# Kernel optimization log

Hardware: AMD Instinct MI355X
Metric: run time of the kernel (lower is better)

## Reference

```python
import jax, jax.numpy as jnp
import numpy as np

N_NODES = 50000
N_EDGES = 640000
IN_FEATS = 512
HID = 128
OUT_FEATS = 128
N_GRAPHS = 256


def setup_inputs() -> dict:
    key = jax.random.key(0)
    ks = jax.random.split(key, 7)
    x = jax.random.normal(ks[0], (N_NODES, IN_FEATS), dtype=jnp.float32)
    edge_index = jax.random.randint(ks[1], (2, N_EDGES), 0, N_NODES, dtype=jnp.int32)
    batch = jnp.sort(jax.random.randint(ks[2], (N_NODES,), 0, N_GRAPHS, dtype=jnp.int32))
    W1 = jax.random.normal(ks[3], (IN_FEATS, HID), dtype=jnp.float32) * (1.0 / np.sqrt(IN_FEATS))
    b1 = jnp.zeros((HID,), jnp.float32)
    W2 = jax.random.normal(ks[4], (HID, OUT_FEATS), dtype=jnp.float32) * (1.0 / np.sqrt(HID))
    b2 = jnp.zeros((OUT_FEATS,), jnp.float32)
    return {"x": x, "W1": W1, "b1": b1, "W2": W2, "b2": b2,
            "edge_index": edge_index, "batch": batch}


def reference(x, W1, b1, W2, b2, edge_index, batch):
    N = x.shape[0]
    loop = jnp.arange(N, dtype=edge_index.dtype)
    # PyG GCNConv default: add self-loops, symmetric deg^-1/2 normalization
    row = jnp.concatenate([edge_index[0], loop])  # source
    col = jnp.concatenate([edge_index[1], loop])  # target
    deg = jax.ops.segment_sum(jnp.ones_like(col, x.dtype), col, num_segments=N)
    dinv = jnp.where(deg > 0, jax.lax.rsqrt(deg), 0.0)
    norm = dinv[row] * dinv[col]  # [E+N]

    def gcn_conv(h, W, b):
        h = h @ W  # linear transform first (PyG order)
        msg = h[row] * norm[:, None]  # gather + scale
        agg = jax.ops.segment_sum(msg, col, num_segments=N)  # scatter-add
        return agg + b

    h = jax.nn.relu(gcn_conv(x, W1, b1))  # dropout is identity in eval mode
    h = gcn_conv(h, W2, b2)
    hs = jax.ops.segment_sum(h, batch, num_segments=N_GRAPHS)  # global_add_pool
    return hs, h
```

## Files before the change

kernel.cpp:

```cpp
#include <hip/hip_runtime.h>
#include <hip/hip_bf16.h>

#define N_NODES  50000
#define N_EDGES  640000
#define IN_FEATS 512
#define HID      128
#define OUT_FEATS 128
#define N_GRAPHS 256

#define SCAN_CHUNK 1024
#define SCAN_BLOCKS ((N_NODES + SCAN_CHUNK - 1) / SCAN_CHUNK)

typedef __attribute__((ext_vector_type(8))) short short8;
typedef __attribute__((ext_vector_type(4))) float f32x4;

__device__ __forceinline__ float bf2f(unsigned u16) {
    return __uint_as_float(u16 << 16);
}
__device__ __forceinline__ unsigned short f2bf(float f) {
    __hip_bfloat16 h = __float2bfloat16(f);
    return *(unsigned short*)&h;
}

#define PREP_BLOCKS 840

__global__ __launch_bounds__(256) void k_prep(const float* __restrict__ W1,
                                              const float* __restrict__ W2,
                                              const int* __restrict__ batch,
                                              unsigned short* __restrict__ wt1,
                                              unsigned short* __restrict__ wt2,
                                              int* __restrict__ cnt,
                                              int* __restrict__ gstart,
                                              float* __restrict__ hs) {
    int b = blockIdx.x;
    int t = threadIdx.x;
    if (b < 196) {
        int i = b * 256 + t;
        if (i < N_NODES) {
            int bt = batch[i];
            int bp = (i == 0) ? -1 : batch[i - 1];
            for (int g = bp + 1; g <= bt; ++g) gstart[g] = i;
            if (i == N_NODES - 1)
                for (int g = bt + 1; g <= N_GRAPHS; ++g) gstart[g] = N_NODES;
        }
    } else if (b < 392) {
        int i = (b - 196) * 256 + t;
        if (i < N_NODES) cnt[i] = 0;
    } else if (b < 648) {
        int idx = (b - 392) * 256 + t;
        int n = idx & 127, k = idx >> 7;
        wt1[(size_t)n * IN_FEATS + k] = f2bf(W1[(size_t)k * 128 + n]);
    } else if (b < 712) {
        int idx = (b - 648) * 256 + t;
        int n = idx & 127, k = idx >> 7;
        wt2[(size_t)n * HID + k] = f2bf(W2[(size_t)k * 128 + n]);
    } else {
        int idx = (b - 712) * 256 + t;
        hs[idx] = 0.f;
    }
}


__global__ void k_count(const int* __restrict__ col, int* __restrict__ cnt) {
    int e4 = (blockIdx.x * blockDim.x + threadIdx.x) * 4;
    if (e4 >= N_EDGES) return;
    int4 c = *(const int4*)(col + e4);
    atomicAdd(&cnt[c.x], 1);
    atomicAdd(&cnt[c.y], 1);
    atomicAdd(&cnt[c.z], 1);
    atomicAdd(&cnt[c.w], 1);
}

__global__ __launch_bounds__(256) void k_scan_a(const int* __restrict__ cnt,
                                                int* __restrict__ offs,
                                                int* __restrict__ bsum) {
    __shared__ int sums[256];
    int t = threadIdx.x;
    int base = blockIdx.x * SCAN_CHUNK + t * 4;
    int c0 = 0, c1 = 0, c2 = 0, c3 = 0;
    if (base + 3 < N_NODES) {
        int4 v = *(const int4*)(cnt + base);
        c0 = v.x; c1 = v.y; c2 = v.z; c3 = v.w;
    } else {
        if (base + 0 < N_NODES) c0 = cnt[base + 0];
        if (base + 1 < N_NODES) c1 = cnt[base + 1];
        if (base + 2 < N_NODES) c2 = cnt[base + 2];
    }
    int ts = c0 + c1 + c2 + c3;
    sums[t] = ts;
    __syncthreads();
#pragma unroll
    for (int off = 1; off < 256; off <<= 1) {
        int add = (t >= off) ? sums[t - off] : 0;
        __syncthreads();
        sums[t] += add;
        __syncthreads();
    }
    int ex = sums[t] - ts;
    if (base + 3 < N_NODES) {
        int4 o;
        o.x = ex; o.y = ex + c0; o.z = ex + c0 + c1; o.w = ex + c0 + c1 + c2;
        *(int4*)(offs + base) = o;
    } else {
        if (base + 0 < N_NODES) offs[base + 0] = ex;
        if (base + 1 < N_NODES) offs[base + 1] = ex + c0;
        if (base + 2 < N_NODES) offs[base + 2] = ex + c0 + c1;
    }
    if (t == 255) bsum[blockIdx.x] = sums[255];
}

__global__ __launch_bounds__(256) void k_scan_c(const int* __restrict__ cnt,
                                                const int* __restrict__ bsum,
                                                int* __restrict__ offs,
                                                int* __restrict__ cursor,
                                                float* __restrict__ dinv) {
    __shared__ int sb[64];
    int t = threadIdx.x;
    int b = blockIdx.x;
    if (t < 64) sb[t] = (t < SCAN_BLOCKS) ? bsum[t] : 0;
    __syncthreads();
#pragma unroll
    for (int off = 1; off < 64; off <<= 1) {
        int add = 0;
        if (t < 64 && t >= off) add = sb[t - off];
        __syncthreads();
        if (t < 64) sb[t] += add;
        __syncthreads();
    }
    int add = (b == 0) ? 0 : sb[b - 1];
    int base = b * SCAN_CHUNK + t * 4;
    if (base + 3 < N_NODES) {
        int4 o = *(const int4*)(offs + base);
        o.x += add; o.y += add; o.z += add; o.w += add;
        *(int4*)(offs + base) = o;
        *(int4*)(cursor + base) = o;
        int4 c = *(const int4*)(cnt + base);
        float4 d;
        d.x = rsqrtf((float)c.x + 1.0f);
        d.y = rsqrtf((float)c.y + 1.0f);
        d.z = rsqrtf((float)c.z + 1.0f);
        d.w = rsqrtf((float)c.w + 1.0f);
        *(float4*)(dinv + base) = d;
    } else {
#pragma unroll
        for (int j = 0; j < 4; ++j) {
            int i = base + j;
            if (i < N_NODES) {
                int o = offs[i] + add;
                offs[i] = o; cursor[i] = o;
                dinv[i] = rsqrtf((float)cnt[i] + 1.0f);
            }
        }
    }
    if (b == 0 && t == 0) offs[N_NODES] = N_EDGES;
}

__global__ void k_fill(const int* __restrict__ row, const int* __restrict__ col,
                       int* __restrict__ cursor, int* __restrict__ srcIdx) {
    int e4 = (blockIdx.x * blockDim.x + threadIdx.x) * 4;
    if (e4 >= N_EDGES) return;
    int4 r = *(const int4*)(row + e4);
    int4 c = *(const int4*)(col + e4);
    srcIdx[atomicAdd(&cursor[c.x], 1)] = r.x;
    srcIdx[atomicAdd(&cursor[c.y], 1)] = r.y;
    srcIdx[atomicAdd(&cursor[c.z], 1)] = r.z;
    srcIdx[atomicAdd(&cursor[c.w], 1)] = r.w;
}


template <int K>
__global__ __launch_bounds__(256) void k_gemm1(const float* __restrict__ A,
                                               const unsigned short* __restrict__ Bt,
                                               unsigned short* __restrict__ Cb, int M) {
    __shared__ unsigned short As[4][128][8];
    __shared__ unsigned short Bs[4][128][8];
    int tid = threadIdx.x;
    int wave = tid >> 6;
    int lane = tid & 63;
    int quad = lane >> 4;
    int l15 = lane & 15;
    int m0 = blockIdx.x * 128;
    int mw = (wave >> 1) * 64;
    int nw = (wave & 1) * 64;

    f32x4 acc[4][4];
#pragma unroll
    for (int i = 0; i < 4; ++i)
#pragma unroll
        for (int j = 0; j < 4; ++j) acc[i][j] = (f32x4){0.f, 0.f, 0.f, 0.f};

    int r0s = tid >> 2, kq0 = tid & 3;
    int r1s = r0s + 64;
    int gm0 = m0 + r0s; if (gm0 >= M) gm0 = M - 1;
    int gm1 = m0 + r1s; if (gm1 >= M) gm1 = M - 1;
    const float* ap0 = A + (size_t)gm0 * K + kq0 * 8;
    const float* ap1 = A + (size_t)gm1 * K + kq0 * 8;

    for (int k0 = 0; k0 < K; k0 += 32) {
        {
            float4 v0 = *(const float4*)(ap0 + k0);
            float4 v1 = *(const float4*)(ap0 + k0 + 4);
            float f[8] = {v0.x, v0.y, v0.z, v0.w, v1.x, v1.y, v1.z, v1.w};
            short8 pk;
#pragma unroll
            for (int j = 0; j < 8; ++j) pk[j] = (short)f2bf(f[j]);
            *(short8*)&As[kq0][r0s][0] = pk;
            v0 = *(const float4*)(ap1 + k0);
            v1 = *(const float4*)(ap1 + k0 + 4);
            float g[8] = {v0.x, v0.y, v0.z, v0.w, v1.x, v1.y, v1.z, v1.w};
#pragma unroll
            for (int j = 0; j < 8; ++j) pk[j] = (short)f2bf(g[j]);
            *(short8*)&As[kq0][r1s][0] = pk;
        }
#pragma unroll
        for (int i = 0; i < 2; ++i) {
            int slot = tid + i * 256;
            int n = slot >> 2, kq = slot & 3;
            *(short8*)&Bs[kq][n][0] = *(const short8*)(Bt + (size_t)n * K + k0 + kq * 8);
        }
        __syncthreads();
        short8 af[4], bfr[4];
#pragma unroll
        for (int i = 0; i < 4; ++i) af[i] = *(short8*)&As[quad][mw + i * 16 + l15][0];
#pragma unroll
        for (int j = 0; j < 4; ++j) bfr[j] = *(short8*)&Bs[quad][nw + j * 16 + l15][0];
#pragma unroll
        for (int i = 0; i < 4; ++i)
#pragma unroll
            for (int j = 0; j < 4; ++j)
                acc[i][j] = __builtin_amdgcn_mfma_f32_16x16x32_bf16(af[i], bfr[j], acc[i][j], 0, 0, 0);
        __syncthreads();
    }
#pragma unroll
    for (int i = 0; i < 4; ++i) {
        int rb = m0 + mw + i * 16 + quad * 4;
#pragma unroll
        for (int j = 0; j < 4; ++j) {
            int colb = nw + j * 16 + l15;
#pragma unroll
            for (int r2 = 0; r2 < 4; ++r2) {
                int gm = rb + r2;
                if (gm < M) Cb[(size_t)gm * 128 + colb] = f2bf(acc[i][j][r2]);
            }
        }
    }
}


__global__ __launch_bounds__(256) void k_gemm2_pool(const unsigned short* __restrict__ G,
                                                    const unsigned short* __restrict__ Bt,
                                                    const float* __restrict__ bias,
                                                    const int* __restrict__ batch,
                                                    float* __restrict__ out,
                                                    float* __restrict__ hs, int M) {
    const int K = HID;
    __shared__ unsigned short As[4][64][8];
    __shared__ unsigned short Bs[4][128][8];
    int tid = threadIdx.x;
    int wave = tid >> 6;
    int lane = tid & 63;
    int quad = lane >> 4;
    int l15 = lane & 15;
    int m0 = blockIdx.x * 64;

    f32x4 acc[8];
#pragma unroll
    for (int nt = 0; nt < 8; ++nt) acc[nt] = (f32x4){0.f, 0.f, 0.f, 0.f};

    int gm_a = m0 + lane; if (gm_a >= M) gm_a = M - 1;
    const unsigned short* ap_base = G + (size_t)gm_a * K + wave * 8;

    for (int k0 = 0; k0 < K; k0 += 32) {
        *(short8*)&As[wave][lane][0] = *(const short8*)(ap_base + k0);
#pragma unroll
        for (int i = 0; i < 2; ++i) {
            int slot = tid + i * 256;
            int bkq = slot >> 7;
            int n = slot & 127;
            *(short8*)&Bs[bkq][n][0] = *(const short8*)(Bt + (size_t)n * K + k0 + bkq * 8);
        }
        __syncthreads();
        short8 a = *(short8*)&As[quad][wave * 16 + l15][0];
#pragma unroll
        for (int nt = 0; nt < 8; ++nt) {
            short8 b = *(short8*)&Bs[quad][nt * 16 + l15][0];
            acc[nt] = __builtin_amdgcn_mfma_f32_16x16x32_bf16(a, b, acc[nt], 0, 0, 0);
        }
        __syncthreads();
    }
    int rb = m0 + wave * 16 + quad * 4;
    int g_[4];
#pragma unroll
    for (int r2 = 0; r2 < 4; ++r2)
        g_[r2] = (rb + r2 < M) ? batch[rb + r2] : -1;
#pragma unroll
    for (int nt = 0; nt < 8; ++nt) {
        int colb = nt * 16 + l15;
        float bcol = bias[colb];
        float v[4];
#pragma unroll
        for (int r2 = 0; r2 < 4; ++r2) {
            v[r2] = acc[nt][r2] + bcol;
            if (rb + r2 < M) out[(size_t)(rb + r2) * 128 + colb] = v[r2];
        }
        float run = v[0];
        int gcur = g_[0];
#pragma unroll
        for (int r2 = 1; r2 < 4; ++r2) {
            if (g_[r2] == gcur) run += v[r2];
            else {
                if (gcur >= 0) atomicAdd(&hs[(size_t)gcur * 128 + colb], run);
                gcur = g_[r2]; run = v[r2];
            }
        }
        if (gcur >= 0) atomicAdd(&hs[(size_t)gcur * 128 + colb], run);
    }
}


template <int RELU, int OUTBF>
__global__ __launch_bounds__(128) void k_agg(const unsigned* __restrict__ t,
                                             const int* __restrict__ offs,
                                             const int* __restrict__ srcIdx,
                                             const float* __restrict__ dinv,
                                             const float* __restrict__ bias,
                                             void* __restrict__ out_) {
    int wave = threadIdx.x >> 6;
    int lane = threadIdx.x & 63;
    int i = blockIdx.x * 2 + wave;
    float di = dinv[i];
    unsigned self = t[(size_t)i * 64 + lane];
    float s0 = bf2f(self & 0xffffu) * di;
    float s1 = bf2f(self >> 16) * di;
    int lo = offs[i], hi = offs[i + 1];
    int e = lo;
    for (; e + 8 <= hi; e += 8) {
        int idx[8];
#pragma unroll
        for (int j = 0; j < 8; ++j) idx[j] = srcIdx[e + j];
        unsigned v[8];
#pragma unroll
        for (int j = 0; j < 8; ++j) v[j] = t[(size_t)idx[j] * 64 + lane];
        float d[8];
#pragma unroll
        for (int j = 0; j < 8; ++j) d[j] = dinv[idx[j]];
#pragma unroll
        for (int j = 0; j < 8; ++j) {
            s0 = fmaf(bf2f(v[j] & 0xffffu), d[j], s0);
            s1 = fmaf(bf2f(v[j] >> 16), d[j], s1);
        }
    }
    for (; e < hi; ++e) {
        int sn = srcIdx[e];
        unsigned vv = t[(size_t)sn * 64 + lane];
        float dd = dinv[sn];
        s0 = fmaf(bf2f(vv & 0xffffu), dd, s0);
        s1 = fmaf(bf2f(vv >> 16), dd, s1);
    }
    float r0 = s0 * di;
    float r1 = s1 * di;
    if (bias) {
        float2 bb = *(const float2*)(bias + lane * 2);
        r0 += bb.x; r1 += bb.y;
    }
    if (RELU) { r0 = fmaxf(r0, 0.f); r1 = fmaxf(r1, 0.f); }
    if (OUTBF) {
        unsigned o = (unsigned)f2bf(r0) | ((unsigned)f2bf(r1) << 16);
        ((unsigned*)out_)[(size_t)i * 64 + lane] = o;
    } else {
        *(float2*)((float*)out_ + (size_t)i * 128 + lane * 2) = make_float2(r0, r1);
    }
}


extern "C" void kernel_launch(void* const* d_in, const int* in_sizes, int n_in,
                              void* d_out, int out_size, void* d_ws, size_t ws_size,
                              hipStream_t stream) {
    const float* x  = (const float*)d_in[0];
    const float* W1 = (const float*)d_in[1];
    const float* b1 = (const float*)d_in[2];
    const float* W2 = (const float*)d_in[3];
    const float* b2 = (const float*)d_in[4];
    const int*   ei = (const int*)d_in[5];
    const int*   batch = (const int*)d_in[6];
    const int* row = ei;
    const int* col = ei + N_EDGES;

    float* out_hs = (float*)d_out;
    float* out_h  = (float*)d_out + N_GRAPHS * OUT_FEATS;

    char* ws = (char*)d_ws;
    unsigned short* tb   = (unsigned short*)ws;
    unsigned short* h1b  = (unsigned short*)(ws + 12800000);
    unsigned short* gb   = (unsigned short*)(ws + 25600000);
    float* dinv = (float*)(ws + 38400000);
    int*   cnt    = (int*)(ws + 38600000);
    int*   offs   = (int*)(ws + 38800000);
    int*   cursor = (int*)(ws + 39000016);
    int*   srcIdx = (int*)(ws + 39200016);
    int*   gstart = (int*)(ws + 41760016);
    int*   bsum   = (int*)(ws + 41761056);
    unsigned short* wt1 = (unsigned short*)(ws + 41761472);
    unsigned short* wt2 = (unsigned short*)(ws + 41892544);

    const int TB = 256;
    k_prep<<<PREP_BLOCKS, 256, 0, stream>>>(W1, W2, batch, wt1, wt2, cnt, gstart, out_hs);
    k_count<<<(N_EDGES / 4 + TB - 1) / TB, TB, 0, stream>>>(col, cnt);
    k_scan_a<<<SCAN_BLOCKS, 256, 0, stream>>>(cnt, offs, bsum);
    k_scan_c<<<SCAN_BLOCKS, 256, 0, stream>>>(cnt, bsum, offs, cursor, dinv);
    k_fill<<<(N_EDGES / 4 + TB - 1) / TB, TB, 0, stream>>>(row, col, cursor, srcIdx);

    k_gemm1<IN_FEATS><<<(N_NODES + 127) / 128, 256, 0, stream>>>(x, wt1, tb, N_NODES);
    k_agg<1, 1><<<N_NODES / 2, 128, 0, stream>>>((const unsigned*)tb, offs, srcIdx, dinv, b1, h1b);
    k_agg<0, 1><<<N_NODES / 2, 128, 0, stream>>>((const unsigned*)h1b, offs, srcIdx, dinv, nullptr, gb);
    k_gemm2_pool<<<(N_NODES + 63) / 64, 256, 0, stream>>>(gb, wt2, b2, batch, out_h, out_hs, N_NODES);
}
```

Baseline: 345.6 us.

## Fuse edge counting into GEMM1 launch and split aggregation across half-waves

The edge degree-count kernel is merged into the first GEMM launch as extra blocks, so the atomic counting runs alongside the matmul instead of as a separate launch. The aggregation kernel is rewritten so each half-wave processes alternate edges with 8-byte loads (4 features per lane), then combines the halves with a cross-lane shuffle. This gives more independent gathers in flight per node, and blocks grow to 4 nodes. The unused gstart computation is dropped from the prep kernel. Padded edge slots load the node's own row with zero weight, which adds some wasted gather traffic for nodes with low degree.

```diff
diff --git a/kernel.cpp b/kernel.cpp
--- a/kernel.cpp
+++ b/kernel.cpp
@@ -22,54 +22,127 @@
     return *(unsigned short*)&h;
 }
 
-#define PREP_BLOCKS 840
+#define PREP_BLOCKS 644
 
 __global__ __launch_bounds__(256) void k_prep(const float* __restrict__ W1,
                                               const float* __restrict__ W2,
-                                              const int* __restrict__ batch,
                                               unsigned short* __restrict__ wt1,
                                               unsigned short* __restrict__ wt2,
                                               int* __restrict__ cnt,
-                                              int* __restrict__ gstart,
                                               float* __restrict__ hs) {
     int b = blockIdx.x;
     int t = threadIdx.x;
     if (b < 196) {
         int i = b * 256 + t;
-        if (i < N_NODES) {
-            int bt = batch[i];
-            int bp = (i == 0) ? -1 : batch[i - 1];
-            for (int g = bp + 1; g <= bt; ++g) gstart[g] = i;
-            if (i == N_NODES - 1)
-                for (int g = bt + 1; g <= N_GRAPHS; ++g) gstart[g] = N_NODES;
-        }
-    } else if (b < 392) {
-        int i = (b - 196) * 256 + t;
         if (i < N_NODES) cnt[i] = 0;
-    } else if (b < 648) {
-        int idx = (b - 392) * 256 + t;
+    } else if (b < 452) {
+        int idx = (b - 196) * 256 + t;
         int n = idx & 127, k = idx >> 7;
         wt1[(size_t)n * IN_FEATS + k] = f2bf(W1[(size_t)k * 128 + n]);
-    } else if (b < 712) {
-        int idx = (b - 648) * 256 + t;
+    } else if (b < 516) {
+        int idx = (b - 452) * 256 + t;
         int n = idx & 127, k = idx >> 7;
         wt2[(size_t)n * HID + k] = f2bf(W2[(size_t)k * 128 + n]);
     } else {
-        int idx = (b - 712) * 256 + t;
+        int idx = (b - 516) * 256 + t;
         hs[idx] = 0.f;
     }
 }
 
 
-__global__ void k_count(const int* __restrict__ col, int* __restrict__ cnt) {
-    int e4 = (blockIdx.x * blockDim.x + threadIdx.x) * 4;
-    if (e4 >= N_EDGES) return;
-    int4 c = *(const int4*)(col + e4);
-    atomicAdd(&cnt[c.x], 1);
-    atomicAdd(&cnt[c.y], 1);
-    atomicAdd(&cnt[c.z], 1);
-    atomicAdd(&cnt[c.w], 1);
-}
+template <int K>
+__global__ __launch_bounds__(256) void k_g1c(const float* __restrict__ A,
+                                             const unsigned short* __restrict__ Bt,
+                                             unsigned short* __restrict__ Cb, int M,
+                                             const int* __restrict__ col,
+                                             int* __restrict__ cnt, int nblk_gemm) {
+    __shared__ unsigned short As[4][128][8];
+    __shared__ unsigned short Bs[4][128][8];
+    int tid = threadIdx.x;
+
+    if (blockIdx.x >= nblk_gemm) {
+        int e4 = ((blockIdx.x - nblk_gemm) * 256 + tid) * 4;
+        if (e4 < N_EDGES) {
+            int4 c = *(const int4*)(col + e4);
+            atomicAdd(&cnt[c.x], 1);
+            atomicAdd(&cnt[c.y], 1);
+            atomicAdd(&cnt[c.z], 1);
+            atomicAdd(&cnt[c.w], 1);
+        }
+        return;
+    }
+
+    int wave = tid >> 6;
+    int lane = tid & 63;
+    int quad = lane >> 4;
+    int l15 = lane & 15;
+    int m0 = blockIdx.x * 128;
+    int mw = (wave >> 1) * 64;
+    int nw = (wave & 1) * 64;
+
+    f32x4 acc[4][4];
+#pragma unroll
+    for (int i = 0; i < 4; ++i)
+#pragma unroll
+        for (int j = 0; j < 4; ++j) acc[i][j] = (f32x4){0.f, 0.f, 0.f, 0.f};
+
+    int r0s = tid >> 2, kq0 = tid & 3;
+    int r1s = r0s + 64;
+    int gm0 = m0 + r0s; if (gm0 >= M) gm0 = M - 1;
+    int gm1 = m0 + r1s; if (gm1 >= M) gm1 = M - 1;
+    const float* ap0 = A + (size_t)gm0 * K + kq0 * 8;
+    const float* ap1 = A + (size_t)gm1 * K + kq0 * 8;
+
+    for (int k0 = 0; k0 < K; k0 += 32) {
+        {
+            float4 v0 = *(const float4*)(ap0 + k0);
+            float4 v1 = *(const float4*)(ap0 + k0 + 4);
+            float f[8] = {v0.x, v0.y, v0.z, v0.w, v1.x, v1.y, v1.z, v1.w};
+            short8 pk;
+#pragma unroll
+            for (int j = 0; j < 8; ++j) pk[j] = (short)f2bf(f[j]);
+            *(short8*)&As[kq0][r0s][0] = pk;
+            v0 = *(const float4*)(ap1 + k0);
+            v1 = *(const float4*)(ap1 + k0 + 4);
+            float g[8] = {v0.x, v0.y, v0.z, v0.w, v1.x, v1.y, v1.z, v1.w};
+#pragma unroll
+            for (int j = 0; j < 8; ++j) pk[j] = (short)f2bf(g[j]);
+            *(short8*)&As[kq0][r1s][0] = pk;
+        }
+#pragma unroll
+        for (int i = 0; i < 2; ++i) {
+            int slot = tid + i * 256;
+            int n = slot >> 2, kq = slot & 3;
+            *(short8*)&Bs[kq][n][0] = *(const short8*)(Bt + (size_t)n * K + k0 + kq * 8);
+        }
+        __syncthreads();
+        short8 af[4], bfr[4];
+#pragma unroll
+        for (int i = 0; i < 4; ++i) af[i] = *(short8*)&As[quad][mw + i * 16 + l15][0];
+#pragma unroll
+        for (int j = 0; j < 4; ++j) bfr[j] = *(short8*)&Bs[quad][nw + j * 16 + l15][0];
+#pragma unroll
+        for (int i = 0; i < 4; ++i)
+#pragma unroll
+            for (int j = 0; j < 4; ++j)
+                acc[i][j] = __builtin_amdgcn_mfma_f32_16x16x32_bf16(af[i], bfr[j], acc[i][j], 0, 0, 0);
+        __syncthreads();
+    }
+#pragma unroll
+    for (int i = 0; i < 4; ++i) {
+        int rb = m0 + mw + i * 16 + quad * 4;
+#pragma unroll
+        for (int j = 0; j < 4; ++j) {
+            int colb = nw + j * 16 + l15;
+#pragma unroll
+            for (int r2 = 0; r2 < 4; ++r2) {
+                int gm = rb + r2;
+                if (gm < M) Cb[(size_t)gm * 128 + colb] = f2bf(acc[i][j][r2]);
+            }
+        }
+    }
+}
+
 
 __global__ __launch_bounds__(256) void k_scan_a(const int* __restrict__ cnt,
                                                 int* __restrict__ offs,
@@ -168,81 +241,76 @@
 }
 
 
-template <int K>
-__global__ __launch_bounds__(256) void k_gemm1(const float* __restrict__ A,
-                                               const unsigned short* __restrict__ Bt,
-                                               unsigned short* __restrict__ Cb, int M) {
-    __shared__ unsigned short As[4][128][8];
-    __shared__ unsigned short Bs[4][128][8];
-    int tid = threadIdx.x;
-    int wave = tid >> 6;
-    int lane = tid & 63;
-    int quad = lane >> 4;
-    int l15 = lane & 15;
-    int m0 = blockIdx.x * 128;
-    int mw = (wave >> 1) * 64;
-    int nw = (wave & 1) * 64;
-
-    f32x4 acc[4][4];
-#pragma unroll
-    for (int i = 0; i < 4; ++i)
-#pragma unroll
-        for (int j = 0; j < 4; ++j) acc[i][j] = (f32x4){0.f, 0.f, 0.f, 0.f};
-
-    int r0s = tid >> 2, kq0 = tid & 3;
-    int r1s = r0s + 64;
-    int gm0 = m0 + r0s; if (gm0 >= M) gm0 = M - 1;
-    int gm1 = m0 + r1s; if (gm1 >= M) gm1 = M - 1;
-    const float* ap0 = A + (size_t)gm0 * K + kq0 * 8;
-    const float* ap1 = A + (size_t)gm1 * K + kq0 * 8;
-
-    for (int k0 = 0; k0 < K; k0 += 32) {
-        {
-            float4 v0 = *(const float4*)(ap0 + k0);
-            float4 v1 = *(const float4*)(ap0 + k0 + 4);
-            float f[8] = {v0.x, v0.y, v0.z, v0.w, v1.x, v1.y, v1.z, v1.w};
-            short8 pk;
-#pragma unroll
-            for (int j = 0; j < 8; ++j) pk[j] = (short)f2bf(f[j]);
-            *(short8*)&As[kq0][r0s][0] = pk;
-            v0 = *(const float4*)(ap1 + k0);
-            v1 = *(const float4*)(ap1 + k0 + 4);
-            float g[8] = {v0.x, v0.y, v0.z, v0.w, v1.x, v1.y, v1.z, v1.w};
-#pragma unroll
-            for (int j = 0; j < 8; ++j) pk[j] = (short)f2bf(g[j]);
-            *(short8*)&As[kq0][r1s][0] = pk;
-        }
-#pragma unroll
-        for (int i = 0; i < 2; ++i) {
-            int slot = tid + i * 256;
-            int n = slot >> 2, kq = slot & 3;
-            *(short8*)&Bs[kq][n][0] = *(const short8*)(Bt + (size_t)n * K + k0 + kq * 8);
-        }
-        __syncthreads();
-        short8 af[4], bfr[4];
-#pragma unroll
-        for (int i = 0; i < 4; ++i) af[i] = *(short8*)&As[quad][mw + i * 16 + l15][0];
-#pragma unroll
-        for (int j = 0; j < 4; ++j) bfr[j] = *(short8*)&Bs[quad][nw + j * 16 + l15][0];
-#pragma unroll
-        for (int i = 0; i < 4; ++i)
-#pragma unroll
-            for (int j = 0; j < 4; ++j)
-                acc[i][j] = __builtin_amdgcn_mfma_f32_16x16x32_bf16(af[i], bfr[j], acc[i][j], 0, 0, 0);
-        __syncthreads();
-    }
-#pragma unroll
-    for (int i = 0; i < 4; ++i) {
-        int rb = m0 + mw + i * 16 + quad * 4;
-#pragma unroll
-        for (int j = 0; j < 4; ++j) {
-            int colb = nw + j * 16 + l15;
-#pragma unroll
-            for (int r2 = 0; r2 < 4; ++r2) {
-                int gm = rb + r2;
-                if (gm < M) Cb[(size_t)gm * 128 + colb] = f2bf(acc[i][j][r2]);
-            }
-        }
+template <int RELU>
+__global__ __launch_bounds__(256) void k_agg(const unsigned* __restrict__ t,
+                                             const int* __restrict__ offs,
+                                             const int* __restrict__ srcIdx,
+                                             const float* __restrict__ dinv,
+                                             const float* __restrict__ bias,
+                                             unsigned* __restrict__ out_) {
+    int wave = threadIdx.x >> 6;
+    int lane = threadIdx.x & 63;
+    int h = lane >> 5;
+    int l = lane & 31;
+    int i = blockIdx.x * 4 + wave;
+    float di = dinv[i];
+    const unsigned* my = t + (size_t)i * 64 + 2 * l;
+
+    float s0 = 0.f, s1 = 0.f, s2 = 0.f, s3 = 0.f;
+    {
+        uint2 sv = *(const uint2*)my;
+        if (h == 0) {
+            s0 = bf2f(sv.x & 0xffffu) * di;
+            s1 = bf2f(sv.x >> 16) * di;
+            s2 = bf2f(sv.y & 0xffffu) * di;
+            s3 = bf2f(sv.y >> 16) * di;
+        }
+    }
+    int lo = offs[i], hi = offs[i + 1];
+    for (int e = lo; e < hi; e += 16) {
+        int idx[8];
+        float d[8];
+        uint2 v[8];
+#pragma unroll
+        for (int j = 0; j < 8; ++j) {
+            int ee = e + 2 * j + h;
+            idx[j] = (ee < hi) ? srcIdx[ee] : i;
+        }
+#pragma unroll
+        for (int j = 0; j < 8; ++j)
+            v[j] = *(const uint2*)(t + (size_t)idx[j] * 64 + 2 * l);
+#pragma unroll
+        for (int j = 0; j < 8; ++j) {
+            int ee = e + 2 * j + h;
+            d[j] = (ee < hi) ? dinv[idx[j]] : 0.f;
+        }
+#pragma unroll
+        for (int j = 0; j < 8; ++j) {
+            s0 = fmaf(bf2f(v[j].x & 0xffffu), d[j], s0);
+            s1 = fmaf(bf2f(v[j].x >> 16),     d[j], s1);
+            s2 = fmaf(bf2f(v[j].y & 0xffffu), d[j], s2);
+            s3 = fmaf(bf2f(v[j].y >> 16),     d[j], s3);
+        }
+    }
+    s0 += __shfl_xor(s0, 32);
+    s1 += __shfl_xor(s1, 32);
+    s2 += __shfl_xor(s2, 32);
+    s3 += __shfl_xor(s3, 32);
+
+    float r0 = s0 * di, r1 = s1 * di, r2 = s2 * di, r3 = s3 * di;
+    if (bias) {
+        float4 bb = *(const float4*)(bias + 4 * l);
+        r0 += bb.x; r1 += bb.y; r2 += bb.z; r3 += bb.w;
+    }
+    if (RELU) {
+        r0 = fmaxf(r0, 0.f); r1 = fmaxf(r1, 0.f);
+        r2 = fmaxf(r2, 0.f); r3 = fmaxf(r3, 0.f);
+    }
+    if (h == 0) {
+        uint2 o;
+        o.x = (unsigned)f2bf(r0) | ((unsigned)f2bf(r1) << 16);
+        o.y = (unsigned)f2bf(r2) | ((unsigned)f2bf(r3) << 16);
+        *(uint2*)(out_ + (size_t)i * 64 + 2 * l) = o;
     }
 }
 
@@ -318,61 +386,6 @@
 }
 
 
-template <int RELU, int OUTBF>
-__global__ __launch_bounds__(128) void k_agg(const unsigned* __restrict__ t,
-                                             const int* __restrict__ offs,
-                                             const int* __restrict__ srcIdx,
-                                             const float* __restrict__ dinv,
-                                             const float* __restrict__ bias,
-                                             void* __restrict__ out_) {
-    int wave = threadIdx.x >> 6;
-    int lane = threadIdx.x & 63;
-    int i = blockIdx.x * 2 + wave;
-    float di = dinv[i];
-    unsigned self = t[(size_t)i * 64 + lane];
-    float s0 = bf2f(self & 0xffffu) * di;
-    float s1 = bf2f(self >> 16) * di;
-    int lo = offs[i], hi = offs[i + 1];
-    int e = lo;
-    for (; e + 8 <= hi; e += 8) {
-        int idx[8];
-#pragma unroll
-        for (int j = 0; j < 8; ++j) idx[j] = srcIdx[e + j];
-        unsigned v[8];
-#pragma unroll
-        for (int j = 0; j < 8; ++j) v[j] = t[(size_t)idx[j] * 64 + lane];
-        float d[8];
-#pragma unroll
-        for (int j = 0; j < 8; ++j) d[j] = dinv[idx[j]];
-#pragma unroll
-        for (int j = 0; j < 8; ++j) {
-            s0 = fmaf(bf2f(v[j] & 0xffffu), d[j], s0);
-            s1 = fmaf(bf2f(v[j] >> 16), d[j], s1);
-        }
-    }
-    for (; e < hi; ++e) {
-        int sn = srcIdx[e];
-        unsigned vv = t[(size_t)sn * 64 + lane];
-        float dd = dinv[sn];
-        s0 = fmaf(bf2f(vv & 0xffffu), dd, s0);
-        s1 = fmaf(bf2f(vv >> 16), dd, s1);
-    }
-    float r0 = s0 * di;
-    float r1 = s1 * di;
-    if (bias) {
-        float2 bb = *(const float2*)(bias + lane * 2);
-        r0 += bb.x; r1 += bb.y;
-    }
-    if (RELU) { r0 = fmaxf(r0, 0.f); r1 = fmaxf(r1, 0.f); }
-    if (OUTBF) {
-        unsigned o = (unsigned)f2bf(r0) | ((unsigned)f2bf(r1) << 16);
-        ((unsigned*)out_)[(size_t)i * 64 + lane] = o;
-    } else {
-        *(float2*)((float*)out_ + (size_t)i * 128 + lane * 2) = make_float2(r0, r1);
-    }
-}
-
-
 extern "C" void kernel_launch(void* const* d_in, const int* in_sizes, int n_in,
                               void* d_out, int out_size, void* d_ws, size_t ws_size,
                               hipStream_t stream) {
@@ -398,20 +411,21 @@
     int*   offs   = (int*)(ws + 38800000);
     int*   cursor = (int*)(ws + 39000016);
     int*   srcIdx = (int*)(ws + 39200016);
-    int*   gstart = (int*)(ws + 41760016);
     int*   bsum   = (int*)(ws + 41761056);
     unsigned short* wt1 = (unsigned short*)(ws + 41761472);
     unsigned short* wt2 = (unsigned short*)(ws + 41892544);
 
     const int TB = 256;
-    k_prep<<<PREP_BLOCKS, 256, 0, stream>>>(W1, W2, batch, wt1, wt2, cnt, gstart, out_hs);
-    k_count<<<(N_EDGES / 4 + TB - 1) / TB, TB, 0, stream>>>(col, cnt);
+    const int GB1 = (N_NODES + 127) / 128;
+    const int CB  = (N_EDGES / 4 + TB - 1) / TB;
+
+    k_prep<<<PREP_BLOCKS, 256, 0, stream>>>(W1, W2, wt1, wt2, cnt, out_hs);
+    k_g1c<IN_FEATS><<<GB1 + CB, 256, 0, stream>>>(x, wt1, tb, N_NODES, col, cnt, GB1);
     k_scan_a<<<SCAN_BLOCKS, 256, 0, stream>>>(cnt, offs, bsum);
     k_scan_c<<<SCAN_BLOCKS, 256, 0, stream>>>(cnt, bsum, offs, cursor, dinv);
     k_fill<<<(N_EDGES / 4 + TB - 1) / TB, TB, 0, stream>>>(row, col, cursor, srcIdx);
 
-    k_gemm1<IN_FEATS><<<(N_NODES + 127) / 128, 256, 0, stream>>>(x, wt1, tb, N_NODES);
-    k_agg<1, 1><<<N_NODES / 2, 128, 0, stream>>>((const unsigned*)tb, offs, srcIdx, dinv, b1, h1b);
-    k_agg<0, 1><<<N_NODES / 2, 128, 0, stream>>>((const unsigned*)h1b, offs, srcIdx, dinv, nullptr, gb);
+    k_agg<1><<<N_NODES / 4, 256, 0, stream>>>((const unsigned*)tb, offs, srcIdx, dinv, b1, (unsigned*)h1b);
+    k_agg<0><<<N_NODES / 4, 256, 0, stream>>>((const unsigned*)h1b, offs, srcIdx, dinv, nullptr, (unsigned*)gb);
     k_gemm2_pool<<<(N_NODES + 63) / 64, 256, 0, stream>>>(gb, wt2, b2, batch, out_h, out_hs, N_NODES);
 }
```

New measurement: 328.0 us. 1.05x faster.
